# Kernel tuning notes

Measured on AMD Instinct MI355X. Metric: run time of the kernel, lower is better.

Reference implementation:

```python
import jax, jax.numpy as jnp
import numpy as np

HIDDEN = 4096
N_HEADS = 32
N_KV_HEADS = 8
HEAD_DIM = HIDDEN // N_HEADS  # 128
GROUPS = N_HEADS // N_KV_HEADS  # 4
ROPE_BASE = 10000.0
BATCH, SEQ = 1, 2048


def _rope_cos_sin(position_ids, dim, base):
    # position_ids: [b, s] int -> cos/sin [b, s, dim]
    inv_freq = 1.0 / (base ** (jnp.arange(0, dim, 2, dtype=jnp.float32) / dim))  # [dim/2]
    freqs = position_ids.astype(jnp.float32)[..., None] * inv_freq  # [b, s, dim/2]
    emb = jnp.concatenate([freqs, freqs], axis=-1)  # [b, s, dim]
    return jnp.cos(emb), jnp.sin(emb)


def _rotate_half(x):
    x1, x2 = jnp.split(x, 2, axis=-1)
    return jnp.concatenate([-x2, x1], axis=-1)


def setup_inputs() -> dict:
    key = jax.random.key(0)
    ks = jax.random.split(key, 8)
    s = 0.02
    return {
        'hidden_states': jax.random.normal(ks[0], (BATCH, SEQ, HIDDEN), dtype=jnp.float32),
        'position_ids': jnp.broadcast_to(jnp.arange(SEQ, dtype=jnp.int64), (BATCH, SEQ)),
        'Wq': jax.random.normal(ks[1], (HIDDEN, N_HEADS * HEAD_DIM), dtype=jnp.float32) * s,
        'bq': jax.random.normal(ks[2], (N_HEADS * HEAD_DIM,), dtype=jnp.float32) * s,
        'Wk': jax.random.normal(ks[3], (HIDDEN, N_KV_HEADS * HEAD_DIM), dtype=jnp.float32) * s,
        'bk': jax.random.normal(ks[4], (N_KV_HEADS * HEAD_DIM,), dtype=jnp.float32) * s,
        'Wv': jax.random.normal(ks[5], (HIDDEN, N_KV_HEADS * HEAD_DIM), dtype=jnp.float32) * s,
        'bv': jax.random.normal(ks[6], (N_KV_HEADS * HEAD_DIM,), dtype=jnp.float32) * s,
        'Wo': jax.random.normal(ks[7], (HIDDEN, HIDDEN), dtype=jnp.float32) * s,
    }


def reference(hidden_states, position_ids, Wq, bq, Wk, bk, Wv, bv, Wo):
    b, s, _ = hidden_states.shape
    # QKV projections (bias=True for q/k/v per module)
    q = hidden_states @ Wq + bq  # [b, s, H*d]
    k = hidden_states @ Wk + bk  # [b, s, Hk*d]
    v = hidden_states @ Wv + bv  # [b, s, Hk*d]
    q = q.reshape(b, s, N_HEADS, HEAD_DIM)
    k = k.reshape(b, s, N_KV_HEADS, HEAD_DIM)
    v = v.reshape(b, s, N_KV_HEADS, HEAD_DIM)

    # RoPE gathered by position_ids
    cos, sin = _rope_cos_sin(position_ids, HEAD_DIM, ROPE_BASE)  # [b, s, d]
    cos = cos[:, :, None, :]
    sin = sin[:, :, None, :]
    q = q * cos + _rotate_half(q) * sin
    k = k * cos + _rotate_half(k) * sin

    # GQA causal attention: group query heads over shared kv heads
    qg = q.reshape(b, s, N_KV_HEADS, GROUPS, HEAD_DIM)
    scale = 1.0 / jnp.sqrt(jnp.asarray(HEAD_DIM, dtype=q.dtype))
    scores = jnp.einsum('bqhgd,bkhd->bhgqk', qg, k) * scale  # [b, Hk, g, s, s]
    causal = jnp.tril(jnp.ones((s, s), dtype=bool))
    scores = jnp.where(causal, scores, jnp.finfo(scores.dtype).min)
    probs = jax.nn.softmax(scores, axis=-1)
    out = jnp.einsum('bhgqk,bkhd->bqhgd', probs, v)  # [b, s, Hk, g, d]
    out = out.reshape(b, s, HIDDEN)
    return out @ Wo  # o_proj, bias=False
```

## Files before the change

### kernel.cpp

```cpp
#include <hip/hip_runtime.h>
#include <hip/hip_bf16.h>

typedef __hip_bfloat16 bf16;
typedef __attribute__((ext_vector_type(8))) __bf16 bf16x8;
typedef __attribute__((ext_vector_type(4))) float f32x4;

#define SEQ 2048
#define HID 4096
#define NH 32
#define NKV 8
#define HD 128
#define KVDIM 1024
#define QKVN 6144

#define MiB (1024 * 1024)

__device__ __forceinline__ void gl_lds16(const void* g, void* lds) {
  __builtin_amdgcn_global_load_lds((const __attribute__((address_space(1))) void*)g,
                                   (__attribute__((address_space(3))) void*)lds,
                                   16, 0, 0);
}

__global__ void cvt_kernel(const float* __restrict__ in, bf16* __restrict__ out, int n) {
  int i = (blockIdx.x * blockDim.x + threadIdx.x) * 4;
  if (i >= n) return;
  float4 v = *reinterpret_cast<const float4*>(in + i);
  bf16 o[4] = {__float2bfloat16(v.x), __float2bfloat16(v.y),
               __float2bfloat16(v.z), __float2bfloat16(v.w)};
  *reinterpret_cast<short4*>(out + i) = *reinterpret_cast<const short4*>(o);
}

__global__ void concat_bias_kernel(const float* __restrict__ bq, const float* __restrict__ bk,
                                   const float* __restrict__ bv, float* __restrict__ o) {
  int i = blockIdx.x * blockDim.x + threadIdx.x;
  if (i >= QKVN) return;
  o[i] = (i < HID) ? bq[i] : (i < HID + KVDIM ? bk[i - HID] : bv[i - HID - KVDIM]);
}

__global__ void transpose_all_kernel(const float* __restrict__ Wq, const float* __restrict__ Wk,
                                     const float* __restrict__ Wv, const float* __restrict__ Wo,
                                     bf16* __restrict__ Wqkvt, bf16* __restrict__ Wot) {
  __shared__ float tile[32][33];
  int t = blockIdx.x;
  const float* in;
  bf16* out;
  int si, xt, yt;
  if (t < 16384)      { in = Wq; out = Wqkvt;                           si = HID;   xt = t & 127; yt = t >> 7; }
  else if (t < 20480) { t -= 16384; in = Wk; out = Wqkvt + (size_t)HID * HID;           si = KVDIM; xt = t & 31; yt = t >> 5; }
  else if (t < 24576) { t -= 20480; in = Wv; out = Wqkvt + (size_t)(HID + KVDIM) * HID; si = KVDIM; xt = t & 31; yt = t >> 5; }
  else                { t -= 24576; in = Wo; out = Wot;                 si = HID;   xt = t & 127; yt = t >> 7; }
  int c0 = xt * 32, r0 = yt * 32;
  int tx = threadIdx.x, ty = threadIdx.y;
#pragma unroll
  for (int i = 0; i < 32; i += 8)
    tile[ty + i][tx] = in[(size_t)(r0 + ty + i) * si + (c0 + tx)];
  __syncthreads();
#pragma unroll
  for (int i = 0; i < 32; i += 8)
    out[(size_t)(c0 + ty + i) * HID + (r0 + tx)] = __float2bfloat16(tile[tx][ty + i]);
}

__global__ void transpose_cvt_kernel(const float* __restrict__ in, bf16* __restrict__ out,
                                     int si, int so) {
  __shared__ float tile[32][33];
  int c0 = blockIdx.x * 32, r0 = blockIdx.y * 32;
  int tx = threadIdx.x, ty = threadIdx.y;
#pragma unroll
  for (int i = 0; i < 32; i += 8)
    tile[ty + i][tx] = in[(size_t)(r0 + ty + i) * si + (c0 + tx)];
  __syncthreads();
#pragma unroll
  for (int i = 0; i < 32; i += 8)
    out[(size_t)(c0 + ty + i) * so + (r0 + tx)] = __float2bfloat16(tile[tx][ty + i]);
}

__global__ void rope_cvt_kernel(const float* __restrict__ in, bf16* __restrict__ out,
                                int nheads, int hshift, int si) {
  int idx = blockIdx.x * blockDim.x + threadIdx.x;
  int i = idx & 63;
  int h = (idx >> 6) & (nheads - 1);
  int s = idx >> (6 + hshift);
  if (s >= SEQ) return;
  float inv = __expf(-(float)i * 0.14391156831212787f);
  float ang = (float)s * inv;
  float sn, cs;
  __sincosf(ang, &sn, &cs);
  size_t bi = (size_t)s * si + (size_t)h * HD + i;
  size_t bo = (size_t)s * ((size_t)nheads * HD) + (size_t)h * HD + i;
  float x1 = in[bi], x2 = in[bi + 64];
  out[bo]      = __float2bfloat16(x1 * cs - x2 * sn);
  out[bo + 64] = __float2bfloat16(x2 * cs + x1 * sn);
}

#define BARRIER() __builtin_amdgcn_s_barrier()
#define LGKM0()                                          \
  {                                                      \
    asm volatile("s_waitcnt lgkmcnt(0)" ::: "memory");   \
    __builtin_amdgcn_sched_barrier(0);                   \
  }
#define MFMA_ACC(d, x, y) d = __builtin_amdgcn_mfma_f32_16x16x32_bf16(x, y, d, 0, 0, 0)

__global__ __launch_bounds__(512, 2) void gemm256_kernel(
    const bf16* __restrict__ A, const bf16* __restrict__ Bt,
    const float* __restrict__ bias, float* __restrict__ C0, float* __restrict__ C1,
    int N, int Ksub, int lda) {
  __shared__ bf16 lds[2][4][128 * 64];
  const int tid = threadIdx.x;
  const int lane = tid & 63;
  const int w = tid >> 6;
  const int wr = w >> 2, wc = w & 3;
  const int m0 = blockIdx.y * 256;
  const int n0 = blockIdx.x * 256;
  const int bz = blockIdx.z;
  const bf16* Ab = A + (size_t)bz * Ksub;
  const bf16* Btb = Bt + (size_t)bz * Ksub;
  float* Cb = bz ? C1 : C0;
  const int nt = Ksub >> 6;

#define STAGE(buf, half, t)                                                     \
  {                                                                             \
    const bf16* _s = ((half) < 2) ? Ab : Btb;                                   \
    int _g0 = (((half) < 2) ? m0 : n0) + ((half) & 1) * 128;                    \
    _Pragma("unroll")                                                           \
    for (int _it = 0; _it < 2; ++_it) {                                         \
      int _row = w * 16 + _it * 8 + (lane >> 3);                                \
      int _ch = (lane & 7) ^ (_row & 7);                                        \
      gl_lds16(_s + (size_t)(_g0 + _row) * lda + (size_t)(t) * 64 + _ch * 8,    \
               &lds[buf][half][(w * 16 + _it * 8) * 64]);                       \
    }                                                                           \
  }

  auto rdA = [&](int cur, int mi, int ks) {
    int rr = mi * 16 + (lane & 15);
    int byt = rr * 128 + (((ks * 32 + (lane >> 4) * 8) * 2) ^ ((rr & 7) << 4));
    return *reinterpret_cast<const bf16x8*>(
        reinterpret_cast<const char*>(&lds[cur][wr][0]) + byt);
  };
  auto rdB = [&](int cur, int ni, int ks) {
    int rr = (wc & 1) * 64 + ni * 16 + (lane & 15);
    int byt = rr * 128 + (((ks * 32 + (lane >> 4) * 8) * 2) ^ ((rr & 7) << 4));
    return *reinterpret_cast<const bf16x8*>(
        reinterpret_cast<const char*>(&lds[cur][2 + (wc >> 1)][0]) + byt);
  };

  f32x4 acc[8][4];
  const f32x4 z = {0.f, 0.f, 0.f, 0.f};
#pragma unroll
  for (int i = 0; i < 8; ++i)
#pragma unroll
    for (int j = 0; j < 4; ++j) acc[i][j] = z;

  STAGE(0, 0, 0); STAGE(0, 1, 0); STAGE(0, 2, 0); STAGE(0, 3, 0);
  STAGE(1, 2, 1); STAGE(1, 3, 1); STAGE(1, 0, 1);
  asm volatile("s_waitcnt vmcnt(6)" ::: "memory");
  BARRIER();

  bf16x8 a[4][2], b[4][2];
  int cur = 0;
  for (int t = 0; t < nt; ++t, cur ^= 1) {
#pragma unroll
    for (int mi = 0; mi < 4; ++mi) { a[mi][0] = rdA(cur, mi, 0); a[mi][1] = rdA(cur, mi, 1); }
#pragma unroll
    for (int ni = 0; ni < 2; ++ni) { b[ni][0] = rdB(cur, ni, 0); b[ni][1] = rdB(cur, ni, 1); }
    if (t + 1 < nt) STAGE(cur ^ 1, 1, t + 1);
    BARRIER();
    LGKM0();
    __builtin_amdgcn_s_setprio(1);
#pragma unroll
    for (int mi = 0; mi < 4; ++mi)
#pragma unroll
      for (int ni = 0; ni < 2; ++ni) {
        MFMA_ACC(acc[mi][ni], a[mi][0], b[ni][0]);
        MFMA_ACC(acc[mi][ni], a[mi][1], b[ni][1]);
      }
    __builtin_amdgcn_s_setprio(0);
    BARRIER();
#pragma unroll
    for (int ni = 2; ni < 4; ++ni) { b[ni][0] = rdB(cur, ni, 0); b[ni][1] = rdB(cur, ni, 1); }
    BARRIER();
    LGKM0();
    __builtin_amdgcn_s_setprio(1);
#pragma unroll
    for (int mi = 0; mi < 4; ++mi)
#pragma unroll
      for (int ni = 2; ni < 4; ++ni) {
        MFMA_ACC(acc[mi][ni], a[mi][0], b[ni][0]);
        MFMA_ACC(acc[mi][ni], a[mi][1], b[ni][1]);
      }
    __builtin_amdgcn_s_setprio(0);
    BARRIER();
#pragma unroll
    for (int mi = 0; mi < 4; ++mi) { a[mi][0] = rdA(cur, mi + 4, 0); a[mi][1] = rdA(cur, mi + 4, 1); }
    if (t + 2 < nt) { STAGE(cur, 2, t + 2); STAGE(cur, 3, t + 2); }
    BARRIER();
    LGKM0();
    __builtin_amdgcn_s_setprio(1);
#pragma unroll
    for (int mi = 0; mi < 4; ++mi)
#pragma unroll
      for (int ni = 2; ni < 4; ++ni) {
        MFMA_ACC(acc[mi + 4][ni], a[mi][0], b[ni][0]);
        MFMA_ACC(acc[mi + 4][ni], a[mi][1], b[ni][1]);
      }
    __builtin_amdgcn_s_setprio(0);
    BARRIER();
    if (t + 2 < nt) STAGE(cur, 0, t + 2);
    if (t + 2 < nt) {
      asm volatile("s_waitcnt vmcnt(6)" ::: "memory");
    } else if (t + 1 < nt) {
      asm volatile("s_waitcnt vmcnt(0)" ::: "memory");
    }
    BARRIER();
    __builtin_amdgcn_s_setprio(1);
#pragma unroll
    for (int mi = 0; mi < 4; ++mi)
#pragma unroll
      for (int ni = 0; ni < 2; ++ni) {
        MFMA_ACC(acc[mi + 4][ni], a[mi][0], b[ni][0]);
        MFMA_ACC(acc[mi + 4][ni], a[mi][1], b[ni][1]);
      }
    __builtin_amdgcn_s_setprio(0);
    BARRIER();
  }

#pragma unroll
  for (int ni = 0; ni < 4; ++ni) {
    int col = n0 + wc * 64 + ni * 16 + (lane & 15);
    float bv = bias ? bias[col] : 0.0f;
#pragma unroll
    for (int mi = 0; mi < 8; ++mi) {
      int rbase = m0 + wr * 128 + mi * 16 + (lane >> 4) * 4;
#pragma unroll
      for (int r = 0; r < 4; ++r)
        Cb[(size_t)(rbase + r) * N + col] = acc[mi][ni][r] + bv;
    }
  }
#undef STAGE
}

__global__ void reduce_kernel(const float* __restrict__ P0, const float* __restrict__ P1,
                              float* __restrict__ out, int n) {
  int i = (blockIdx.x * blockDim.x + threadIdx.x) * 4;
  if (i >= n) return;
  float4 a = *reinterpret_cast<const float4*>(P0 + i);
  float4 b = *reinterpret_cast<const float4*>(P1 + i);
  float4 o = {a.x + b.x, a.y + b.y, a.z + b.z, a.w + b.w};
  *reinterpret_cast<float4*>(out + i) = o;
}

__global__ __launch_bounds__(256) void attn_kernel(
    const bf16* __restrict__ Q,
    const bf16* __restrict__ Kb,
    const bf16* __restrict__ Vt,
    bf16* __restrict__ AO,
    float* __restrict__ Opart,
    float* __restrict__ Ml) {
  __shared__ bf16 Ks[64 * 128];
  __shared__ bf16 Vs[128 * 64];
  __shared__ bf16 Ps[4][16 * 64];
  const int tid = threadIdx.x, lane = tid & 63, w = tid >> 6;
  const int b = blockIdx.x;
  const int H = b & 31;
  const int tt = b >> 5;
  int qb, lo, hi, half;
  bool split;
  if (tt < 32) {
    qb = 16 + ((31 - tt) >> 1);
    half = tt & 1;
    int n = qb + 1, mid = n >> 1;
    lo = half ? mid : 0;
    hi = half ? n : mid;
    split = true;
  } else {
    qb = 47 - tt;
    half = 0;
    lo = 0;
    hi = qb + 1;
    split = false;
  }
  const int kvh = H >> 2;
  const int qw = qb * 64 + w * 16;
  const int hig = lane >> 4;
  const int q_loc = lane & 15;
  const int qa = qw + q_loc;

  bf16x8 aq[4];
#pragma unroll
  for (int kd = 0; kd < 4; ++kd) {
    int row = qw + q_loc;
    int d = kd * 32 + hig * 8;
    aq[kd] = *reinterpret_cast<const bf16x8*>(Q + (size_t)row * HID + H * HD + d);
  }

  float m_run = -1e30f, l_run = 0.0f;
  f32x4 o[8];
  const f32x4 z = {0.f, 0.f, 0.f, 0.f};
#pragma unroll
  for (int dt = 0; dt < 8; ++dt) o[dt] = z;

  const float scale = 0.08838834764831845f;

  for (int t = lo; t < hi; ++t) {
    int kvbase = t * 64;
#pragma unroll
    for (int it = 0; it < 4; ++it) {
      int c = w * 4 + it;
      int row = c * 4 + (lane >> 4);
      int sb = ((lane & 15) * 16) ^ ((row & 7) << 4);
      gl_lds16(Kb + (size_t)(kvbase + row) * KVDIM + kvh * HD + (sb >> 1), &Ks[c * 512]);
    }
#pragma unroll
    for (int it = 0; it < 4; ++it) {
      int c = w * 4 + it;
      int row = c * 8 + (lane >> 3);
      int sb = ((lane & 7) * 16) ^ ((row & 7) << 4);
      gl_lds16(Vt + (size_t)(kvh * HD + row) * SEQ + kvbase + (sb >> 1), &Vs[c * 512]);
    }
    __syncthreads();

    f32x4 sf[4];
#pragma unroll
    for (int j = 0; j < 4; ++j) sf[j] = z;
#pragma unroll
    for (int j = 0; j < 4; ++j) {
#pragma unroll
      for (int kd = 0; kd < 4; ++kd) {
        int r = j * 16 + q_loc;
        int byt = r * 256 + (((kd * 32 + hig * 8) * 2) ^ ((r & 7) << 4));
        bf16x8 kfr = *reinterpret_cast<const bf16x8*>(reinterpret_cast<const char*>(Ks) + byt);
        sf[j] = __builtin_amdgcn_mfma_f32_16x16x32_bf16(kfr, aq[kd], sf[j], 0, 0, 0);
      }
    }

    float vals[4][4];
    bool diag = (t == qb);
#pragma unroll
    for (int j = 0; j < 4; ++j)
#pragma unroll
      for (int r = 0; r < 4; ++r) {
        float v = sf[j][r] * scale;
        if (diag) {
          int ka = kvbase + j * 16 + hig * 4 + r;
          if (ka > qa) v = -1e30f;
        }
        vals[j][r] = v;
      }

    float m01 = fmaxf(fmaxf(vals[0][0], vals[0][1]), fmaxf(vals[0][2], vals[0][3]));
    float m23 = fmaxf(fmaxf(vals[1][0], vals[1][1]), fmaxf(vals[1][2], vals[1][3]));
    float m45 = fmaxf(fmaxf(vals[2][0], vals[2][1]), fmaxf(vals[2][2], vals[2][3]));
    float m67 = fmaxf(fmaxf(vals[3][0], vals[3][1]), fmaxf(vals[3][2], vals[3][3]));
    float m = fmaxf(fmaxf(m01, m23), fmaxf(m45, m67));
    m = fmaxf(m, __shfl_xor(m, 16));
    m = fmaxf(m, __shfl_xor(m, 32));
    float mn = fmaxf(m_run, m);
    float alpha = __expf(m_run - mn);
    m_run = mn;

    float p[4][4];
    float rs = 0.0f;
#pragma unroll
    for (int j = 0; j < 4; ++j)
#pragma unroll
      for (int r = 0; r < 4; ++r) {
        p[j][r] = __expf(vals[j][r] - mn);
        rs += p[j][r];
      }
    rs += __shfl_xor(rs, 16);
    rs += __shfl_xor(rs, 32);
    l_run = l_run * alpha + rs;

#pragma unroll
    for (int j = 0; j < 4; ++j) {
      bf16 tmp[4] = {__float2bfloat16(p[j][0]), __float2bfloat16(p[j][1]),
                     __float2bfloat16(p[j][2]), __float2bfloat16(p[j][3])};
      int coff = (j * 16 + hig * 4) * 2;
      int byt = q_loc * 128 + (coff ^ ((q_loc & 7) << 4));
      *reinterpret_cast<uint2*>(reinterpret_cast<char*>(&Ps[w][0]) + byt) =
          *reinterpret_cast<const uint2*>(tmp);
    }

#pragma unroll
    for (int r = 0; r < 4; ++r) {
      float alr = __shfl(alpha, hig * 4 + r);
#pragma unroll
      for (int dt = 0; dt < 8; ++dt) o[dt][r] *= alr;
    }

    bf16x8 pa[2];
#pragma unroll
    for (int ks = 0; ks < 2; ++ks) {
      int byt = q_loc * 128 + (((ks * 32 + hig * 8) * 2) ^ ((q_loc & 7) << 4));
      pa[ks] = *reinterpret_cast<const bf16x8*>(reinterpret_cast<const char*>(&Ps[w][0]) + byt);
    }
#pragma unroll
    for (int dt = 0; dt < 8; ++dt)
#pragma unroll
      for (int ks = 0; ks < 2; ++ks) {
        int vrow = dt * 16 + q_loc;
        int byt = vrow * 128 + (((ks * 32 + hig * 8) * 2) ^ ((vrow & 7) << 4));
        bf16x8 vb = *reinterpret_cast<const bf16x8*>(reinterpret_cast<const char*>(Vs) + byt);
        o[dt] = __builtin_amdgcn_mfma_f32_16x16x32_bf16(pa[ks], vb, o[dt], 0, 0, 0);
      }
    __syncthreads();
  }

  if (!split) {
#pragma unroll
    for (int r = 0; r < 4; ++r) {
      float li = __shfl(l_run, hig * 4 + r);
      float linv = 1.0f / li;
#pragma unroll
      for (int dt = 0; dt < 8; ++dt) {
        int qrow = qw + hig * 4 + r;
        int d = dt * 16 + q_loc;
        AO[(size_t)qrow * HID + H * HD + d] = __float2bfloat16(o[dt][r] * linv);
      }
    }
  } else {
    size_t pbase = ((size_t)(half * NH + H) * 1024);
#pragma unroll
    for (int dt = 0; dt < 8; ++dt)
#pragma unroll
      for (int r = 0; r < 4; ++r) {
        int qrow = qw + hig * 4 + r;
        int d = dt * 16 + q_loc;
        Opart[(pbase + (qrow - 1024)) * HD + d] = o[dt][r];
      }
    if (lane < 16) {
      Ml[(pbase + (qa - 1024)) * 2 + 0] = m_run;
      Ml[(pbase + (qa - 1024)) * 2 + 1] = l_run;
    }
  }
}

__global__ __launch_bounds__(256) void merge_kernel(
    const float* __restrict__ Opart, const float* __restrict__ Ml,
    bf16* __restrict__ AO) {
  int i = blockIdx.x * 256 + threadIdx.x;
  int dq = (i & 31) << 2;
  int row = (i >> 5) & 1023;
  int H = i >> 15;
  size_t b1 = (size_t)H * 1024 + row;
  size_t b2 = (size_t)(NH + H) * 1024 + row;
  float m1 = Ml[b1 * 2], l1 = Ml[b1 * 2 + 1];
  float m2 = Ml[b2 * 2], l2 = Ml[b2 * 2 + 1];
  float M = fmaxf(m1, m2);
  float w1 = __expf(m1 - M), w2 = __expf(m2 - M);
  float inv = 1.0f / (l1 * w1 + l2 * w2);
  float4 o1 = *reinterpret_cast<const float4*>(Opart + b1 * HD + dq);
  float4 o2 = *reinterpret_cast<const float4*>(Opart + b2 * HD + dq);
  bf16 o[4] = {__float2bfloat16((o1.x * w1 + o2.x * w2) * inv),
               __float2bfloat16((o1.y * w1 + o2.y * w2) * inv),
               __float2bfloat16((o1.z * w1 + o2.z * w2) * inv),
               __float2bfloat16((o1.w * w1 + o2.w * w2) * inv)};
  *reinterpret_cast<short4*>(AO + (size_t)(1024 + row) * HID + H * HD + dq) =
      *reinterpret_cast<const short4*>(o);
}

extern "C" void kernel_launch(void* const* d_in, const int* in_sizes, int n_in,
                              void* d_out, int out_size, void* d_ws, size_t ws_size,
                              hipStream_t stream) {
  const float* hidden = (const float*)d_in[0];
  const float* Wq = (const float*)d_in[2];
  const float* bq = (const float*)d_in[3];
  const float* Wk = (const float*)d_in[4];
  const float* bk = (const float*)d_in[5];
  const float* Wv = (const float*)d_in[6];
  const float* bv = (const float*)d_in[7];
  const float* Wo = (const float*)d_in[8];
  float* out = (float*)d_out;

  char* ws = (char*)d_ws;
  bf16*  Wqkvt = (bf16*)(ws + (size_t)0 * MiB);
  bf16*  Xb    = (bf16*)(ws + (size_t)48 * MiB);
  float* Cqkv  = (float*)(ws + (size_t)64 * MiB);
  bf16*  Wot   = (bf16*)(ws + (size_t)112 * MiB);
  bf16*  Qb    = (bf16*)(ws + (size_t)144 * MiB);
  bf16*  Kb    = (bf16*)(ws + (size_t)160 * MiB);
  bf16*  Vt    = (bf16*)(ws + (size_t)164 * MiB);
  float* bqkv  = (float*)Qb;
  bf16*  AO    = (bf16*)Cqkv;
  float* Opart = (float*)Wqkvt;
  float* Ml    = (float*)(ws + (size_t)32 * MiB);
  float* P0    = (float*)Wqkvt;
  float* P1    = (float*)(ws + (size_t)80 * MiB);

  cvt_kernel<<<(SEQ * HID) / 1024, 256, 0, stream>>>(hidden, Xb, SEQ * HID);
  concat_bias_kernel<<<QKVN / 256, 256, 0, stream>>>(bq, bk, bv, bqkv);
  transpose_all_kernel<<<40960, dim3(32, 8), 0, stream>>>(Wq, Wk, Wv, Wo, Wqkvt, Wot);

  gemm256_kernel<<<dim3(QKVN / 256, SEQ / 256, 1), 512, 0, stream>>>(
      Xb, Wqkvt, bqkv, Cqkv, nullptr, QKVN, HID, HID);

  rope_cvt_kernel<<<(SEQ * NH * 64) / 256, 256, 0, stream>>>(Cqkv, Qb, NH, 5, QKVN);
  rope_cvt_kernel<<<(SEQ * NKV * 64) / 256, 256, 0, stream>>>(Cqkv + HID, Kb, NKV, 3, QKVN);
  transpose_cvt_kernel<<<dim3(KVDIM / 32, SEQ / 32), dim3(32, 8), 0, stream>>>(
      Cqkv + HID + KVDIM, Vt, QKVN, SEQ);

  attn_kernel<<<1536, 256, 0, stream>>>(Qb, Kb, Vt, AO, Opart, Ml);
  merge_kernel<<<(NH * 1024 * 32) / 256, 256, 0, stream>>>(Opart, Ml, AO);

  gemm256_kernel<<<dim3(HID / 256, SEQ / 256, 2), 512, 0, stream>>>(
      AO, Wot, nullptr, P0, P1, HID, 2048, HID);
  reduce_kernel<<<(SEQ * HID) / 1024, 256, 0, stream>>>(P0, P1, out, SEQ * HID);
}
```

Measured before the change: 360.0 us.

## Overlap Wo transpose with QKV GEMM, emit bf16 QKV, fuse RoPE/V-transpose

Moves the Wo transpose into extra blocks of the QKV GEMM launch so it runs on otherwise idle CUs alongside the 192 GEMM tiles. The QKV GEMM now writes bf16 output instead of fp32, which halves that write traffic and the traffic read back by the post-processing step. The two RoPE launches and the V transpose are merged into one kernel that processes two elements per thread. The cost is a more complex GEMM kernel with a runtime mode branch, a flattened grid index, and a workspace layout that has been reshuffled.

```diff
diff --git a/kernel.cpp b/kernel.cpp
--- a/kernel.cpp
+++ b/kernel.cpp
@@ -21,6 +21,13 @@
                                    16, 0, 0);
 }
 
+__device__ __forceinline__ float unplo(unsigned u) { return __uint_as_float(u << 16); }
+__device__ __forceinline__ float unphi(unsigned u) { return __uint_as_float(u & 0xffff0000u); }
+__device__ __forceinline__ unsigned packbf(float a, float b) {
+  bf16 t[2] = {__float2bfloat16(a), __float2bfloat16(b)};
+  return *reinterpret_cast<unsigned*>(t);
+}
+
 __global__ void cvt_kernel(const float* __restrict__ in, bf16* __restrict__ out, int n) {
   int i = (blockIdx.x * blockDim.x + threadIdx.x) * 4;
   if (i >= n) return;
@@ -37,9 +44,8 @@
   o[i] = (i < HID) ? bq[i] : (i < HID + KVDIM ? bk[i - HID] : bv[i - HID - KVDIM]);
 }
 
-__global__ void transpose_all_kernel(const float* __restrict__ Wq, const float* __restrict__ Wk,
-                                     const float* __restrict__ Wv, const float* __restrict__ Wo,
-                                     bf16* __restrict__ Wqkvt, bf16* __restrict__ Wot) {
+__global__ void transpose_qkvw_kernel(const float* __restrict__ Wq, const float* __restrict__ Wk,
+                                      const float* __restrict__ Wv, bf16* __restrict__ Wqkvt) {
   __shared__ float tile[32][33];
   int t = blockIdx.x;
   const float* in;
@@ -47,8 +53,7 @@
   int si, xt, yt;
   if (t < 16384)      { in = Wq; out = Wqkvt;                           si = HID;   xt = t & 127; yt = t >> 7; }
   else if (t < 20480) { t -= 16384; in = Wk; out = Wqkvt + (size_t)HID * HID;           si = KVDIM; xt = t & 31; yt = t >> 5; }
-  else if (t < 24576) { t -= 20480; in = Wv; out = Wqkvt + (size_t)(HID + KVDIM) * HID; si = KVDIM; xt = t & 31; yt = t >> 5; }
-  else                { t -= 24576; in = Wo; out = Wot;                 si = HID;   xt = t & 127; yt = t >> 7; }
+  else                { t -= 20480; in = Wv; out = Wqkvt + (size_t)(HID + KVDIM) * HID; si = KVDIM; xt = t & 31; yt = t >> 5; }
   int c0 = xt * 32, r0 = yt * 32;
   int tx = threadIdx.x, ty = threadIdx.y;
 #pragma unroll
@@ -60,36 +65,45 @@
     out[(size_t)(c0 + ty + i) * HID + (r0 + tx)] = __float2bfloat16(tile[tx][ty + i]);
 }
 
-__global__ void transpose_cvt_kernel(const float* __restrict__ in, bf16* __restrict__ out,
-                                     int si, int so) {
+__global__ void postqkv_kernel(const bf16* __restrict__ Ch, bf16* __restrict__ Qb,
+                               bf16* __restrict__ Kb, bf16* __restrict__ Vt) {
   __shared__ float tile[32][33];
-  int c0 = blockIdx.x * 32, r0 = blockIdx.y * 32;
-  int tx = threadIdx.x, ty = threadIdx.y;
-#pragma unroll
-  for (int i = 0; i < 32; i += 8)
-    tile[ty + i][tx] = in[(size_t)(r0 + ty + i) * si + (c0 + tx)];
-  __syncthreads();
-#pragma unroll
-  for (int i = 0; i < 32; i += 8)
-    out[(size_t)(c0 + ty + i) * so + (r0 + tx)] = __float2bfloat16(tile[tx][ty + i]);
-}
-
-__global__ void rope_cvt_kernel(const float* __restrict__ in, bf16* __restrict__ out,
-                                int nheads, int hshift, int si) {
-  int idx = blockIdx.x * blockDim.x + threadIdx.x;
-  int i = idx & 63;
-  int h = (idx >> 6) & (nheads - 1);
-  int s = idx >> (6 + hshift);
-  if (s >= SEQ) return;
-  float inv = __expf(-(float)i * 0.14391156831212787f);
-  float ang = (float)s * inv;
-  float sn, cs;
-  __sincosf(ang, &sn, &cs);
-  size_t bi = (size_t)s * si + (size_t)h * HD + i;
-  size_t bo = (size_t)s * ((size_t)nheads * HD) + (size_t)h * HD + i;
-  float x1 = in[bi], x2 = in[bi + 64];
-  out[bo]      = __float2bfloat16(x1 * cs - x2 * sn);
-  out[bo + 64] = __float2bfloat16(x2 * cs + x1 * sn);
+  int b = blockIdx.x;
+  int tid = threadIdx.x;
+  if (b < 10240) {
+    bool isQ = (b < 8192);
+    int idx = (isQ ? b : b - 8192) * 256 + tid;
+    int j = idx & 31;
+    int h = (idx >> 5) & (isQ ? 31 : 7);
+    int s = idx >> (isQ ? 10 : 8);
+    size_t bi = (size_t)s * QKVN + (isQ ? 0 : HID) + h * HD;
+    unsigned u1 = *reinterpret_cast<const unsigned*>(Ch + bi + 2 * j);
+    unsigned u2 = *reinterpret_cast<const unsigned*>(Ch + bi + 64 + 2 * j);
+    float x1a = unplo(u1), x1b = unphi(u1);
+    float x2a = unplo(u2), x2b = unphi(u2);
+    float inv0 = __expf(-(float)(2 * j) * 0.14391156831212787f);
+    float inv1 = __expf(-(float)(2 * j + 1) * 0.14391156831212787f);
+    float sn0, cs0, sn1, cs1;
+    __sincosf((float)s * inv0, &sn0, &cs0);
+    __sincosf((float)s * inv1, &sn1, &cs1);
+    size_t bo = (size_t)s * (isQ ? HID : KVDIM) + h * HD;
+    bf16* Ob = isQ ? Qb : Kb;
+    *reinterpret_cast<unsigned*>(Ob + bo + 2 * j) =
+        packbf(x1a * cs0 - x2a * sn0, x1b * cs1 - x2b * sn1);
+    *reinterpret_cast<unsigned*>(Ob + bo + 64 + 2 * j) =
+        packbf(x2a * cs0 + x1a * sn0, x2b * cs1 + x1b * sn1);
+  } else {
+    int t = b - 10240;
+    int xt = t & 31, yt = t >> 5;
+    int tx = tid & 31, ty = tid >> 5;
+#pragma unroll
+    for (int i = 0; i < 32; i += 8)
+      tile[ty + i][tx] = __bfloat162float(Ch[(size_t)(yt * 32 + ty + i) * QKVN + (HID + KVDIM) + xt * 32 + tx]);
+    __syncthreads();
+#pragma unroll
+    for (int i = 0; i < 32; i += 8)
+      Vt[(size_t)(xt * 32 + ty + i) * SEQ + (yt * 32 + tx)] = __float2bfloat16(tile[tx][ty + i]);
+  }
 }
 
 #define BARRIER() __builtin_amdgcn_s_barrier()
@@ -103,18 +117,46 @@
 __global__ __launch_bounds__(512, 2) void gemm256_kernel(
     const bf16* __restrict__ A, const bf16* __restrict__ Bt,
     const float* __restrict__ bias, float* __restrict__ C0, float* __restrict__ C1,
-    int N, int Ksub, int lda) {
+    bf16* __restrict__ Ch, const float* __restrict__ WoSrc, bf16* __restrict__ WotDst,
+    int N, int Ksub, int lda, int mode) {
   __shared__ bf16 lds[2][4][128 * 64];
+  const int blk = blockIdx.x;
+  int bx, by, bz;
+  if (mode == 1) {
+    if (blk >= 192) {
+      float (*tile)[32][33] = reinterpret_cast<float(*)[32][33]>(&lds[0][0][0]);
+      int k = blk - 192;
+      int tid = threadIdx.x;
+      int sub = tid >> 8, tx = tid & 31, ty = (tid >> 5) & 7;
+      for (int p = 0; p < 128; ++p) {
+        int t = k * 256 + p * 2 + sub;
+        int xt = t & 127, yt = t >> 7;
+#pragma unroll
+        for (int i = 0; i < 32; i += 8)
+          tile[sub][ty + i][tx] = WoSrc[(size_t)(yt * 32 + ty + i) * HID + xt * 32 + tx];
+        __syncthreads();
+#pragma unroll
+        for (int i = 0; i < 32; i += 8)
+          WotDst[(size_t)(xt * 32 + ty + i) * HID + (yt * 32 + tx)] =
+              __float2bfloat16(tile[sub][tx][ty + i]);
+        __syncthreads();
+      }
+      return;
+    }
+    bx = blk % 24; by = blk / 24; bz = 0;
+  } else {
+    bz = blk >> 7;
+    int rem = blk & 127;
+    bx = rem & 15; by = rem >> 4;
+  }
   const int tid = threadIdx.x;
   const int lane = tid & 63;
   const int w = tid >> 6;
   const int wr = w >> 2, wc = w & 3;
-  const int m0 = blockIdx.y * 256;
-  const int n0 = blockIdx.x * 256;
-  const int bz = blockIdx.z;
+  const int m0 = by * 256;
+  const int n0 = bx * 256;
   const bf16* Ab = A + (size_t)bz * Ksub;
   const bf16* Btb = Bt + (size_t)bz * Ksub;
-  float* Cb = bz ? C1 : C0;
   const int nt = Ksub >> 6;
 
 #define STAGE(buf, half, t)                                                     \
@@ -223,16 +265,31 @@
     BARRIER();
   }
 
-#pragma unroll
-  for (int ni = 0; ni < 4; ++ni) {
-    int col = n0 + wc * 64 + ni * 16 + (lane & 15);
-    float bv = bias ? bias[col] : 0.0f;
-#pragma unroll
-    for (int mi = 0; mi < 8; ++mi) {
-      int rbase = m0 + wr * 128 + mi * 16 + (lane >> 4) * 4;
-#pragma unroll
-      for (int r = 0; r < 4; ++r)
-        Cb[(size_t)(rbase + r) * N + col] = acc[mi][ni][r] + bv;
+  if (mode == 1) {
+#pragma unroll
+    for (int ni = 0; ni < 4; ++ni) {
+      int col = n0 + wc * 64 + ni * 16 + (lane & 15);
+      float bv = bias[col];
+#pragma unroll
+      for (int mi = 0; mi < 8; ++mi) {
+        int rbase = m0 + wr * 128 + mi * 16 + (lane >> 4) * 4;
+#pragma unroll
+        for (int r = 0; r < 4; ++r)
+          Ch[(size_t)(rbase + r) * N + col] = __float2bfloat16(acc[mi][ni][r] + bv);
+      }
+    }
+  } else {
+    float* Cb = bz ? C1 : C0;
+#pragma unroll
+    for (int ni = 0; ni < 4; ++ni) {
+      int col = n0 + wc * 64 + ni * 16 + (lane & 15);
+#pragma unroll
+      for (int mi = 0; mi < 8; ++mi) {
+        int rbase = m0 + wr * 128 + mi * 16 + (lane >> 4) * 4;
+#pragma unroll
+        for (int r = 0; r < 4; ++r)
+          Cb[(size_t)(rbase + r) * N + col] = acc[mi][ni][r];
+      }
     }
   }
 #undef STAGE
@@ -472,36 +529,34 @@
   float* out = (float*)d_out;
 
   char* ws = (char*)d_ws;
-  bf16*  Wqkvt = (bf16*)(ws + (size_t)0 * MiB);
-  bf16*  Xb    = (bf16*)(ws + (size_t)48 * MiB);
-  float* Cqkv  = (float*)(ws + (size_t)64 * MiB);
-  bf16*  Wot   = (bf16*)(ws + (size_t)112 * MiB);
-  bf16*  Qb    = (bf16*)(ws + (size_t)144 * MiB);
-  bf16*  Kb    = (bf16*)(ws + (size_t)160 * MiB);
-  bf16*  Vt    = (bf16*)(ws + (size_t)164 * MiB);
-  float* bqkv  = (float*)Qb;
-  bf16*  AO    = (bf16*)Cqkv;
-  float* Opart = (float*)Wqkvt;
-  float* Ml    = (float*)(ws + (size_t)32 * MiB);
-  float* P0    = (float*)Wqkvt;
-  float* P1    = (float*)(ws + (size_t)80 * MiB);
+  bf16*  Wqkvt  = (bf16*)(ws + (size_t)0 * MiB);
+  bf16*  Xb     = (bf16*)(ws + (size_t)48 * MiB);
+  bf16*  Cqkvh  = (bf16*)(ws + (size_t)64 * MiB);
+  bf16*  Wot    = (bf16*)(ws + (size_t)88 * MiB);
+  bf16*  Qb     = (bf16*)(ws + (size_t)120 * MiB);
+  bf16*  Kb     = (bf16*)(ws + (size_t)136 * MiB);
+  bf16*  Vt     = (bf16*)(ws + (size_t)140 * MiB);
+  float* bqkv   = (float*)Qb;
+  bf16*  AO     = Cqkvh;
+  float* Opart  = (float*)Wqkvt;
+  float* Ml     = (float*)(ws + (size_t)48 * MiB);
+  float* P0     = (float*)Wqkvt;
+  float* P1     = (float*)(ws + (size_t)16 * MiB);
+  P1 = (float*)(ws + (size_t)32 * MiB);
 
   cvt_kernel<<<(SEQ * HID) / 1024, 256, 0, stream>>>(hidden, Xb, SEQ * HID);
   concat_bias_kernel<<<QKVN / 256, 256, 0, stream>>>(bq, bk, bv, bqkv);
-  transpose_all_kernel<<<40960, dim3(32, 8), 0, stream>>>(Wq, Wk, Wv, Wo, Wqkvt, Wot);
-
-  gemm256_kernel<<<dim3(QKVN / 256, SEQ / 256, 1), 512, 0, stream>>>(
-      Xb, Wqkvt, bqkv, Cqkv, nullptr, QKVN, HID, HID);
-
-  rope_cvt_kernel<<<(SEQ * NH * 64) / 256, 256, 0, stream>>>(Cqkv, Qb, NH, 5, QKVN);
-  rope_cvt_kernel<<<(SEQ * NKV * 64) / 256, 256, 0, stream>>>(Cqkv + HID, Kb, NKV, 3, QKVN);
-  transpose_cvt_kernel<<<dim3(KVDIM / 32, SEQ / 32), dim3(32, 8), 0, stream>>>(
-      Cqkv + HID + KVDIM, Vt, QKVN, SEQ);
+  transpose_qkvw_kernel<<<24576, dim3(32, 8), 0, stream>>>(Wq, Wk, Wv, Wqkvt);
+
+  gemm256_kernel<<<256, 512, 0, stream>>>(
+      Xb, Wqkvt, bqkv, nullptr, nullptr, Cqkvh, Wo, Wot, QKVN, HID, HID, 1);
+
+  postqkv_kernel<<<12288, 256, 0, stream>>>(Cqkvh, Qb, Kb, Vt);
 
   attn_kernel<<<1536, 256, 0, stream>>>(Qb, Kb, Vt, AO, Opart, Ml);
   merge_kernel<<<(NH * 1024 * 32) / 256, 256, 0, stream>>>(Opart, Ml, AO);
 
-  gemm256_kernel<<<dim3(HID / 256, SEQ / 256, 2), 512, 0, stream>>>(
-      AO, Wot, nullptr, P0, P1, HID, 2048, HID);
+  gemm256_kernel<<<256, 512, 0, stream>>>(
+      AO, Wot, nullptr, P0, P1, nullptr, nullptr, nullptr, HID, 2048, HID, 0);
   reduce_kernel<<<(SEQ * HID) / 1024, 256, 0, stream>>>(P0, P1, out, SEQ * HID);
 }
```

Measured after the change: 358.0 us. No clear change (-0.5%).
